# Kernel optimization log

Measured on AMD Instinct MI355X. Metric: run time of the kernel, lower is better.

The kernel has to match this reference:

```python
import jax, jax.numpy as jnp
import numpy as np

B, C, H, W = 32, 3, 224, 224
P = 16            # patch size
D = 768           # model dim
L = 12            # depth
HEADS = 12
DH = D // HEADS   # 64
MLP = 3072
NC = 1000
N = (H // P) * (W // P) + 1  # 197 tokens (196 patches + cls)


def setup_inputs() -> dict:
    key = jax.random.key(0)
    ks = iter(jax.random.split(key, 16))
    def rnd(shape, s=0.02):
        return jax.random.normal(next(ks), shape, dtype=jnp.float32) * s
    return dict(
        imgs=jax.random.normal(next(ks), (B, C, H, W), dtype=jnp.float32),
        patch_w=rnd((D, C, P, P)),
        patch_b=jnp.zeros((D,), jnp.float32),
        cls_token=rnd((D,)),
        pos_emb=rnd((N, D)),
        ln1_g=jnp.ones((L, D), jnp.float32), ln1_b=jnp.zeros((L, D), jnp.float32),
        wq=rnd((L, D, D)), bq=jnp.zeros((L, D), jnp.float32),
        wk=rnd((L, D, D)), bk=jnp.zeros((L, D), jnp.float32),
        wv=rnd((L, D, D)), bv=jnp.zeros((L, D), jnp.float32),
        wo=rnd((L, D, D)), bo=jnp.zeros((L, D), jnp.float32),
        ln2_g=jnp.ones((L, D), jnp.float32), ln2_b=jnp.zeros((L, D), jnp.float32),
        w1=rnd((L, D, MLP)), b1=jnp.zeros((L, MLP), jnp.float32),
        w2=rnd((L, MLP, D)), b2=jnp.zeros((L, D), jnp.float32),
        hn_g=jnp.ones((D,), jnp.float32), hn_b=jnp.zeros((D,), jnp.float32),
        hw=rnd((D, NC)), hb=jnp.zeros((NC,), jnp.float32),
    )


def layer_norm(x, g, b, eps=1e-5):
    mu = x.mean(-1, keepdims=True)
    var = ((x - mu) ** 2).mean(-1, keepdims=True)
    return (x - mu) * jax.lax.rsqrt(var + eps) * g + b


def reference(imgs, patch_w, patch_b, cls_token, pos_emb,
              ln1_g, ln1_b, wq, bq, wk, bk, wv, bv, wo, bo,
              ln2_g, ln2_b, w1, b1, w2, b2, hn_g, hn_b, hw, hb):
    # patch embedding: strided conv, NCHW / OIHW
    x = jax.lax.conv_general_dilated(
        imgs, patch_w, window_strides=(P, P), padding='VALID',
        dimension_numbers=('NCHW', 'OIHW', 'NCHW'))
    x = x + patch_b[None, :, None, None]
    x = x.reshape(B, D, -1).transpose(0, 2, 1)          # [B, 196, D]
    cls = jnp.broadcast_to(cls_token, (B, 1, D))        # zeros_like + cls_token
    x = jnp.concatenate([cls, x], axis=1) + pos_emb[:N] # [B, N, D]

    scale = DH ** -0.5
    for i in range(L):
        h = layer_norm(x, ln1_g[i], ln1_b[i])
        q = (h @ wq[i] + bq[i]).reshape(B, N, HEADS, DH)
        k = (h @ wk[i] + bk[i]).reshape(B, N, HEADS, DH)
        v = (h @ wv[i] + bv[i]).reshape(B, N, HEADS, DH)
        att = jax.nn.softmax(jnp.einsum('bnhd,bmhd->bhnm', q, k) * scale, axis=-1)
        o = jnp.einsum('bhnm,bmhd->bnhd', att, v).reshape(B, N, D)
        x = x + (o @ wo[i] + bo[i])
        h = layer_norm(x, ln2_g[i], ln2_b[i])
        x = x + (jax.nn.gelu(h @ w1[i] + b1[i]) @ w2[i] + b2[i])

    x = x.mean(axis=1)                                   # [B, D]
    return layer_norm(x, hn_g, hn_b) @ hw + hb           # [B, NC]
```

## Files before the change

kernel.cpp:

```cpp
#include <hip/hip_runtime.h>
#include <hip/hip_bf16.h>

typedef unsigned short u16;
typedef __bf16 bf16x8 __attribute__((ext_vector_type(8)));
typedef float f32x4 __attribute__((ext_vector_type(4)));

#define BATCH 32
#define NTOK 197
#define DIM 768
#define LAYERS 12
#define HEADS 12
#define DHEAD 64
#define MLPD 3072
#define NCLS 1000
#define SROWS 6304
#define SLD 224

constexpr long OFF_X  = 0;
constexpr long OFF_H  = 19365888;
constexpr long OFF_O  = 29048832;
constexpr long OFF_WB = 38731776;
constexpr long OFF_Q  = 43450368;
constexpr long OFF_K  = 53133312;
constexpr long OFF_VT = 62816256;
constexpr long OFF_S  = 73826304;
constexpr long OFF_PL = OFF_WB;
constexpr long OFF_HB = OFF_WB + 98304;

__device__ inline u16 f2bf(float f) {
    __hip_bfloat16 h = __float2bfloat16(f);
    return __builtin_bit_cast(u16, h);
}
__device__ inline float bf2f(u16 u) {
    unsigned int x = ((unsigned int)u) << 16;
    return __builtin_bit_cast(float, x);
}
__device__ inline void async16(const u16* g, u16* l) {
    __builtin_amdgcn_global_load_lds(
        (const __attribute__((address_space(1))) void*)g,
        (__attribute__((address_space(3))) void*)l, 16, 0, 0);
}

__global__ __launch_bounds__(256) void im2col_kernel(
        const float* __restrict__ imgs, u16* __restrict__ out) {
    int idx = blockIdx.x * 256 + threadIdx.x;
    if (idx >= 6272 * 768) return;
    int col = idx % 768, row = idx / 768;
    int b = row / 196, p = row % 196;
    int py = p / 14, px = p % 14;
    int c = col >> 8, ph = (col >> 4) & 15, pw = col & 15;
    float v = imgs[(((long)b * 3 + c) * 224 + (py * 16 + ph)) * 224 + (px * 16 + pw)];
    out[idx] = f2bf(v);
}

__global__ __launch_bounds__(256) void cast_kernel(
        const float* __restrict__ in, u16* __restrict__ out, int n) {
    int idx = blockIdx.x * 256 + threadIdx.x;
    if (idx < n) out[idx] = f2bf(in[idx]);
}

__global__ __launch_bounds__(256) void transpose_cast(
        const float* __restrict__ in, u16* __restrict__ out, int R, int C) {
    __shared__ float tile[32][33];
    int bx = blockIdx.x * 32;
    int by = blockIdx.y * 32;
    int tx = threadIdx.x & 31, ty = threadIdx.x >> 5;
#pragma unroll
    for (int i = 0; i < 32; i += 8) {
        int r = by + ty + i, c = bx + tx;
        if (r < R && c < C) tile[ty + i][tx] = in[(long)r * C + c];
    }
    __syncthreads();
#pragma unroll
    for (int i = 0; i < 32; i += 8) {
        int c = bx + ty + i, r = by + tx;
        if (r < R && c < C) out[(long)c * R + r] = f2bf(tile[tx][ty + i]);
    }
}

__global__ __launch_bounds__(256) void add_pos_kernel(
        float* __restrict__ x, const float* __restrict__ cls,
        const float* __restrict__ pos) {
    int idx = blockIdx.x * 256 + threadIdx.x;
    if (idx >= SROWS * DIM) return;
    int d = idx % DIM, row = idx / DIM, n = row % NTOK;
    if (n == 0) x[idx] = cls[d] + pos[d];
    else        x[idx] += pos[(long)n * DIM + d];
}

__device__ inline float block_sum(float v, float* red) {
#pragma unroll
    for (int off = 32; off; off >>= 1) v += __shfl_xor(v, off, 64);
    int w = threadIdx.x >> 6;
    if ((threadIdx.x & 63) == 0) red[w] = v;
    __syncthreads();
    float s = red[0] + red[1] + red[2] + red[3];
    __syncthreads();
    return s;
}

__global__ __launch_bounds__(256) void ln_kernel(
        const float* __restrict__ x, const float* __restrict__ g,
        const float* __restrict__ bt, u16* __restrict__ out) {
    __shared__ float red[4];
    long row = blockIdx.x;
    const float* xr = x + row * DIM;
    int t = threadIdx.x;
    float v0 = xr[t], v1 = xr[t + 256], v2 = xr[t + 512];
    float mean = block_sum(v0 + v1 + v2, red) * (1.f / 768.f);
    float d0 = v0 - mean, d1 = v1 - mean, d2 = v2 - mean;
    float var = block_sum(d0 * d0 + d1 * d1 + d2 * d2, red) * (1.f / 768.f);
    float rs = rsqrtf(var + 1e-5f);
    u16* o = out + row * DIM;
    o[t]       = f2bf(d0 * rs * g[t]       + bt[t]);
    o[t + 256] = f2bf(d1 * rs * g[t + 256] + bt[t + 256]);
    o[t + 512] = f2bf(d2 * rs * g[t + 512] + bt[t + 512]);
}

__global__ __launch_bounds__(256) void softmax_rows(u16* __restrict__ S) {
    int row = blockIdx.x * 4 + (threadIdx.x >> 6);
    int lane = threadIdx.x & 63;
    u16* p = S + (long)row * SLD;
    float v[4];
#pragma unroll
    for (int i = 0; i < 4; i++) {
        int c = lane + i * 64;
        v[i] = (c < NTOK) ? bf2f(p[c]) : -1e30f;
    }
    float mx = fmaxf(fmaxf(v[0], v[1]), fmaxf(v[2], v[3]));
#pragma unroll
    for (int off = 32; off; off >>= 1) mx = fmaxf(mx, __shfl_xor(mx, off, 64));
    float s = 0.f;
#pragma unroll
    for (int i = 0; i < 4; i++) {
        v[i] = (v[i] > -1e29f) ? __expf(v[i] - mx) : 0.f;
        s += v[i];
    }
#pragma unroll
    for (int off = 32; off; off >>= 1) s += __shfl_xor(s, off, 64);
    float inv = 1.f / s;
#pragma unroll
    for (int i = 0; i < 4; i++) {
        int c = lane + i * 64;
        if (c < NTOK) p[c] = f2bf(v[i] * inv);
    }
}

__global__ __launch_bounds__(256) void mean_pool_kernel(
        const float* __restrict__ x, float* __restrict__ pooled) {
    int idx = blockIdx.x * 256 + threadIdx.x;
    if (idx >= BATCH * DIM) return;
    int b = idx / DIM, d = idx % DIM;
    float s = 0.f;
    for (int n = 0; n < NTOK; n++) s += x[((long)b * NTOK + n) * DIM + d];
    pooled[idx] = s * (1.f / 197.f);
}

__global__ __launch_bounds__(256) void head_kernel(
        const u16* __restrict__ hx, const float* __restrict__ hw,
        const float* __restrict__ hb, float* __restrict__ out) {
    __shared__ float xr[DIM];
    int b = blockIdx.x;
    for (int i = threadIdx.x; i < DIM; i += 256) xr[i] = bf2f(hx[b * DIM + i]);
    __syncthreads();
    for (int c = threadIdx.x; c < NCLS; c += 256) {
        float s = hb[c];
        for (int d = 0; d < DIM; d++) s += xr[d] * hw[(long)d * NCLS + c];
        out[b * NCLS + c] = s;
    }
}

constexpr int OM_F32 = 0, OM_BF16 = 1, OM_PATCH = 2, OM_QK = 3, OM_VT = 4,
              OM_S = 5, OM_ATTN = 6;
constexpr int EPI_NONE = 0, EPI_GELU = 1;

template<int TM, int TN, int OUT_MODE, int EPI, bool RESID>
__global__ __launch_bounds__(256, 2) void gemm_async(
        const u16* __restrict__ Aall, const u16* __restrict__ Ball,
        void* __restrict__ Cptr, const float* __restrict__ bias,
        int M, int N, int K, int lda, int ldb, int ldc,
        long sA, long sB, float scale) {
    __shared__ u16 As[TM * 32];
    __shared__ u16 Bs[TN * 32];
    int g = blockIdx.z;
    const u16* A = Aall + (long)g * sA;
    const u16* B = Ball + (long)g * sB;
    int m0 = blockIdx.x * TM;
    int n0 = blockIdx.y * TN;
    int tid = threadIdx.x;
    int lane = tid & 63;
    int wave = tid >> 6;
    int wm, wn;
    if (TN == 128) { wm = (wave & 1) * 64; wn = (wave >> 1) * 64; }
    else           { wm = wave * 64;       wn = 0; }
    int lm = lane & 15;
    int lq = lane >> 4;

    f32x4 acc[4][4];
    const f32x4 z4 = {0.f, 0.f, 0.f, 0.f};
#pragma unroll
    for (int i = 0; i < 4; i++)
#pragma unroll
        for (int j = 0; j < 4; j++) acc[i][j] = z4;

    int rsub = lane >> 2;
    int ksub = (lane & 3) * 8;

    for (int k0 = 0; k0 < K; k0 += 32) {
#pragma unroll
        for (int c = 0; c < TM / 64; c++) {
            int row = c * 64 + wave * 16;
            int gr = m0 + row + rsub;
            gr = gr < M ? gr : M - 1;
            async16(A + (long)gr * lda + k0 + ksub, &As[row * 32]);
        }
#pragma unroll
        for (int c = 0; c < TN / 64; c++) {
            int row = c * 64 + wave * 16;
            int gn = n0 + row + rsub;
            gn = gn < N ? gn : N - 1;
            async16(B + (long)gn * ldb + k0 + ksub, &Bs[row * 32]);
        }
        __syncthreads();
        bf16x8 af[4], bfr[4];
#pragma unroll
        for (int i = 0; i < 4; i++)
            af[i] = *reinterpret_cast<const bf16x8*>(&As[(wm + i * 16 + lm) * 32 + lq * 8]);
#pragma unroll
        for (int i = 0; i < 4; i++)
            bfr[i] = *reinterpret_cast<const bf16x8*>(&Bs[(wn + i * 16 + lm) * 32 + lq * 8]);
#pragma unroll
        for (int mi = 0; mi < 4; mi++)
#pragma unroll
            for (int ni = 0; ni < 4; ni++)
                acc[mi][ni] = __builtin_amdgcn_mfma_f32_16x16x32_bf16(
                        af[mi], bfr[ni], acc[mi][ni], 0, 0, 0);
        __syncthreads();
    }

    int nlim = (OUT_MODE == OM_S) ? SLD : N;
#pragma unroll
    for (int mi = 0; mi < 4; mi++) {
#pragma unroll
        for (int ni = 0; ni < 4; ni++) {
#pragma unroll
            for (int r = 0; r < 4; r++) {
                int m = m0 + wm + mi * 16 + lq * 4 + r;
                int n = n0 + wn + ni * 16 + lm;
                if (m < M && n < nlim) {
                    float v = 0.f;
                    if (!(OUT_MODE == OM_S && n >= N)) {
                        v = acc[mi][ni][r] * scale;
                        if (bias) v += bias[n];
                        if (EPI == EPI_GELU) {
                            float u = v;
                            v = 0.5f * u * (1.f + tanhf(0.7978845608028654f *
                                                        (u + 0.044715f * u * u * u)));
                        }
                    }
                    if (OUT_MODE == OM_F32) {
                        float* Cf = (float*)Cptr;
                        long idx = (long)m * ldc + n;
                        if (RESID) v += Cf[idx];
                        Cf[idx] = v;
                    } else if (OUT_MODE == OM_BF16) {
                        ((u16*)Cptr)[(long)m * ldc + n] = f2bf(v);
                    } else if (OUT_MODE == OM_PATCH) {
                        int row = m + m / 196 + 1;
                        ((float*)Cptr)[(long)row * DIM + n] = v;
                    } else if (OUT_MODE == OM_QK) {
                        int b = m / NTOK, tok = m - b * NTOK;
                        int hh = n >> 6, dh = n & 63;
                        ((u16*)Cptr)[((((long)b * HEADS + hh) * NTOK + tok) << 6) + dh] = f2bf(v);
                    } else if (OUT_MODE == OM_VT) {
                        int b = m / NTOK, tok = m - b * NTOK;
                        int hh = n >> 6, dh = n & 63;
                        ((u16*)Cptr)[(((long)b * HEADS + hh) * 64 + dh) * SLD + tok] = f2bf(v);
                    } else if (OUT_MODE == OM_S) {
                        ((u16*)Cptr)[(long)g * (NTOK * SLD) + (long)m * SLD + n] = f2bf(v);
                    } else {
                        int b = g / HEADS, hh = g - b * HEADS;
                        ((u16*)Cptr)[((long)(b * NTOK + m)) * DIM + hh * 64 + n] = f2bf(v);
                    }
                }
            }
        }
    }
}

extern "C" void kernel_launch(void* const* d_in, const int* in_sizes, int n_in,
                              void* d_out, int out_size, void* d_ws, size_t ws_size,
                              hipStream_t stream) {
    const float* imgs    = (const float*)d_in[0];
    const float* patch_w = (const float*)d_in[1];
    const float* patch_b = (const float*)d_in[2];
    const float* cls_tok = (const float*)d_in[3];
    const float* pos_emb = (const float*)d_in[4];
    const float* ln1_g   = (const float*)d_in[5];
    const float* ln1_b   = (const float*)d_in[6];
    const float* wq      = (const float*)d_in[7];
    const float* bq      = (const float*)d_in[8];
    const float* wk      = (const float*)d_in[9];
    const float* bk      = (const float*)d_in[10];
    const float* wv      = (const float*)d_in[11];
    const float* bv      = (const float*)d_in[12];
    const float* wo      = (const float*)d_in[13];
    const float* bo      = (const float*)d_in[14];
    const float* ln2_g   = (const float*)d_in[15];
    const float* ln2_b   = (const float*)d_in[16];
    const float* w1      = (const float*)d_in[17];
    const float* b1      = (const float*)d_in[18];
    const float* w2      = (const float*)d_in[19];
    const float* b2      = (const float*)d_in[20];
    const float* hn_g    = (const float*)d_in[21];
    const float* hn_b    = (const float*)d_in[22];
    const float* hw      = (const float*)d_in[23];
    const float* hbias   = (const float*)d_in[24];

    char* ws = (char*)d_ws;
    float* x     = (float*)(ws + OFF_X);
    u16*   h     = (u16*)(ws + OFF_H);
    u16*   obuf  = (u16*)(ws + OFF_O);
    u16*   wbuf  = (u16*)(ws + OFF_WB);
    u16*   qbuf  = (u16*)(ws + OFF_Q);
    u16*   kbuf  = (u16*)(ws + OFF_K);
    u16*   vtbuf = (u16*)(ws + OFF_VT);
    u16*   Sbuf  = (u16*)(ws + OFF_S);
    u16*   patchA = (u16*)(ws + OFF_Q);
    u16*   mlph   = (u16*)(ws + OFF_Q);
    float* pooled = (float*)(ws + OFF_PL);
    u16*   hb16   = (u16*)(ws + OFF_HB);

    im2col_kernel<<<(6272 * 768 + 255) / 256, 256, 0, stream>>>(imgs, patchA);
    cast_kernel<<<(589824 + 255) / 256, 256, 0, stream>>>(patch_w, wbuf, 589824);
    gemm_async<128, 128, OM_PATCH, EPI_NONE, false><<<dim3(49, 6, 1), 256, 0, stream>>>(
        patchA, wbuf, x, patch_b, 6272, 768, 768, 768, 768, 768, 0, 0, 1.f);
    add_pos_kernel<<<(SROWS * DIM + 255) / 256, 256, 0, stream>>>(x, cls_tok, pos_emb);

    for (int l = 0; l < LAYERS; ++l) {
        const long wstride = (long)DIM * DIM;
        ln_kernel<<<SROWS, 256, 0, stream>>>(x, ln1_g + l * DIM, ln1_b + l * DIM, h);

        transpose_cast<<<dim3(24, 24), 256, 0, stream>>>(wq + l * wstride, wbuf, DIM, DIM);
        gemm_async<128, 128, OM_QK, EPI_NONE, false><<<dim3(50, 6, 1), 256, 0, stream>>>(
            h, wbuf, qbuf, bq + l * DIM, SROWS, DIM, DIM, DIM, DIM, 0, 0, 0, 1.f);
        transpose_cast<<<dim3(24, 24), 256, 0, stream>>>(wk + l * wstride, wbuf, DIM, DIM);
        gemm_async<128, 128, OM_QK, EPI_NONE, false><<<dim3(50, 6, 1), 256, 0, stream>>>(
            h, wbuf, kbuf, bk + l * DIM, SROWS, DIM, DIM, DIM, DIM, 0, 0, 0, 1.f);
        transpose_cast<<<dim3(24, 24), 256, 0, stream>>>(wv + l * wstride, wbuf, DIM, DIM);
        gemm_async<128, 128, OM_VT, EPI_NONE, false><<<dim3(50, 6, 1), 256, 0, stream>>>(
            h, wbuf, vtbuf, bv + l * DIM, SROWS, DIM, DIM, DIM, DIM, 0, 0, 0, 1.f);

        gemm_async<128, 128, OM_S, EPI_NONE, false><<<dim3(2, 2, 384), 256, 0, stream>>>(
            qbuf, kbuf, Sbuf, nullptr, NTOK, NTOK, DHEAD, DHEAD, DHEAD, 0,
            (long)NTOK * DHEAD, (long)NTOK * DHEAD, 0.125f);
        softmax_rows<<<(384 * NTOK) / 4, 256, 0, stream>>>(Sbuf);
        gemm_async<256, 64, OM_ATTN, EPI_NONE, false><<<dim3(1, 1, 384), 256, 0, stream>>>(
            Sbuf, vtbuf, obuf, nullptr, NTOK, DHEAD, SLD, SLD, SLD, 0,
            (long)NTOK * SLD, (long)64 * SLD, 1.f);

        transpose_cast<<<dim3(24, 24), 256, 0, stream>>>(wo + l * wstride, wbuf, DIM, DIM);
        gemm_async<128, 128, OM_F32, EPI_NONE, true><<<dim3(50, 6, 1), 256, 0, stream>>>(
            obuf, wbuf, x, bo + l * DIM, SROWS, DIM, DIM, DIM, DIM, DIM, 0, 0, 1.f);

        ln_kernel<<<SROWS, 256, 0, stream>>>(x, ln2_g + l * DIM, ln2_b + l * DIM, h);
        transpose_cast<<<dim3(96, 24), 256, 0, stream>>>(w1 + (long)l * DIM * MLPD, wbuf, DIM, MLPD);
        gemm_async<128, 128, OM_BF16, EPI_GELU, false><<<dim3(50, 24, 1), 256, 0, stream>>>(
            h, wbuf, mlph, b1 + l * MLPD, SROWS, MLPD, DIM, DIM, DIM, MLPD, 0, 0, 1.f);
        transpose_cast<<<dim3(24, 96), 256, 0, stream>>>(w2 + (long)l * MLPD * DIM, wbuf, MLPD, DIM);
        gemm_async<128, 128, OM_F32, EPI_NONE, true><<<dim3(50, 6, 1), 256, 0, stream>>>(
            mlph, wbuf, x, b2 + l * DIM, SROWS, DIM, MLPD, MLPD, MLPD, DIM, 0, 0, 1.f);
    }

    mean_pool_kernel<<<(BATCH * DIM + 255) / 256, 256, 0, stream>>>(x, pooled);
    ln_kernel<<<BATCH, 256, 0, stream>>>(pooled, hn_g, hn_b, hb16);
    head_kernel<<<BATCH, 256, 0, stream>>>(hb16, hw, hbias, (float*)d_out);
}
```

Before: 5.666 ms.

## Fuse attention into one kernel, merge QKV GEMM and weight transposes

Replaces the separate QK^T GEMM, softmax and PV GEMM with a single attention kernel that keeps scores and probabilities in LDS per 64-query tile, removing the bf16 score buffer round-trip through global memory. Q, K and V projections become one GEMM with N=2304 and a per-segment epilogue, and the four DxD weight transposes run in one launch. The head kernel is also split across more blocks. This cuts launches and memory traffic, at the cost of high LDS use per block (about 70KB) in the attention kernel, which may limit occupancy.

```diff
diff --git a/kernel.cpp b/kernel.cpp
--- a/kernel.cpp
+++ b/kernel.cpp
@@ -15,6 +15,7 @@
 #define NCLS 1000
 #define SROWS 6304
 #define SLD 224
+#define PLD 232
 
 constexpr long OFF_X  = 0;
 constexpr long OFF_H  = 19365888;
@@ -23,9 +24,9 @@
 constexpr long OFF_Q  = 43450368;
 constexpr long OFF_K  = 53133312;
 constexpr long OFF_VT = 62816256;
-constexpr long OFF_S  = 73826304;
 constexpr long OFF_PL = OFF_WB;
 constexpr long OFF_HB = OFF_WB + 98304;
+constexpr long QK_SEG = 4841472;
 
 __device__ inline u16 f2bf(float f) {
     __hip_bfloat16 h = __float2bfloat16(f);
@@ -62,8 +63,7 @@
 __global__ __launch_bounds__(256) void transpose_cast(
         const float* __restrict__ in, u16* __restrict__ out, int R, int C) {
     __shared__ float tile[32][33];
-    int bx = blockIdx.x * 32;
-    int by = blockIdx.y * 32;
+    int bx = blockIdx.x * 32, by = blockIdx.y * 32;
     int tx = threadIdx.x & 31, ty = threadIdx.x >> 5;
 #pragma unroll
     for (int i = 0; i < 32; i += 8) {
@@ -76,6 +76,25 @@
         int c = bx + ty + i, r = by + tx;
         if (r < R && c < C) out[(long)c * R + r] = f2bf(tile[tx][ty + i]);
     }
+}
+
+__global__ __launch_bounds__(256) void transpose_cast4(
+        const float* __restrict__ p0, const float* __restrict__ p1,
+        const float* __restrict__ p2, const float* __restrict__ p3,
+        u16* __restrict__ out) {
+    __shared__ float tile[32][33];
+    int z = blockIdx.z;
+    const float* in = z == 0 ? p0 : z == 1 ? p1 : z == 2 ? p2 : p3;
+    u16* o = out + (long)z * DIM * DIM;
+    int bx = blockIdx.x * 32, by = blockIdx.y * 32;
+    int tx = threadIdx.x & 31, ty = threadIdx.x >> 5;
+#pragma unroll
+    for (int i = 0; i < 32; i += 8)
+        tile[ty + i][tx] = in[(long)(by + ty + i) * DIM + bx + tx];
+    __syncthreads();
+#pragma unroll
+    for (int i = 0; i < 32; i += 8)
+        o[(long)(bx + ty + i) * DIM + by + tx] = f2bf(tile[tx][ty + i]);
 }
 
 __global__ __launch_bounds__(256) void add_pos_kernel(
@@ -117,35 +136,6 @@
     o[t + 512] = f2bf(d2 * rs * g[t + 512] + bt[t + 512]);
 }
 
-__global__ __launch_bounds__(256) void softmax_rows(u16* __restrict__ S) {
-    int row = blockIdx.x * 4 + (threadIdx.x >> 6);
-    int lane = threadIdx.x & 63;
-    u16* p = S + (long)row * SLD;
-    float v[4];
-#pragma unroll
-    for (int i = 0; i < 4; i++) {
-        int c = lane + i * 64;
-        v[i] = (c < NTOK) ? bf2f(p[c]) : -1e30f;
-    }
-    float mx = fmaxf(fmaxf(v[0], v[1]), fmaxf(v[2], v[3]));
-#pragma unroll
-    for (int off = 32; off; off >>= 1) mx = fmaxf(mx, __shfl_xor(mx, off, 64));
-    float s = 0.f;
-#pragma unroll
-    for (int i = 0; i < 4; i++) {
-        v[i] = (v[i] > -1e29f) ? __expf(v[i] - mx) : 0.f;
-        s += v[i];
-    }
-#pragma unroll
-    for (int off = 32; off; off >>= 1) s += __shfl_xor(s, off, 64);
-    float inv = 1.f / s;
-#pragma unroll
-    for (int i = 0; i < 4; i++) {
-        int c = lane + i * 64;
-        if (c < NTOK) p[c] = f2bf(v[i] * inv);
-    }
-}
-
 __global__ __launch_bounds__(256) void mean_pool_kernel(
         const float* __restrict__ x, float* __restrict__ pooled) {
     int idx = blockIdx.x * 256 + threadIdx.x;
@@ -163,36 +153,32 @@
     int b = blockIdx.x;
     for (int i = threadIdx.x; i < DIM; i += 256) xr[i] = bf2f(hx[b * DIM + i]);
     __syncthreads();
-    for (int c = threadIdx.x; c < NCLS; c += 256) {
+    int c = blockIdx.y * 256 + threadIdx.x;
+    if (c < NCLS) {
         float s = hb[c];
         for (int d = 0; d < DIM; d++) s += xr[d] * hw[(long)d * NCLS + c];
         out[b * NCLS + c] = s;
     }
 }
 
-constexpr int OM_F32 = 0, OM_BF16 = 1, OM_PATCH = 2, OM_QK = 3, OM_VT = 4,
-              OM_S = 5, OM_ATTN = 6;
+constexpr int OM_F32 = 0, OM_BF16 = 1, OM_PATCH = 2, OM_QKV = 3;
 constexpr int EPI_NONE = 0, EPI_GELU = 1;
 
-template<int TM, int TN, int OUT_MODE, int EPI, bool RESID>
+template<int OUT_MODE, int EPI, bool RESID>
 __global__ __launch_bounds__(256, 2) void gemm_async(
-        const u16* __restrict__ Aall, const u16* __restrict__ Ball,
+        const u16* __restrict__ A, const u16* __restrict__ B,
         void* __restrict__ Cptr, const float* __restrict__ bias,
-        int M, int N, int K, int lda, int ldb, int ldc,
-        long sA, long sB, float scale) {
-    __shared__ u16 As[TM * 32];
-    __shared__ u16 Bs[TN * 32];
-    int g = blockIdx.z;
-    const u16* A = Aall + (long)g * sA;
-    const u16* B = Ball + (long)g * sB;
-    int m0 = blockIdx.x * TM;
-    int n0 = blockIdx.y * TN;
+        const float* __restrict__ bias2, const float* __restrict__ bias3,
+        int M, int N, int K, int lda, int ldb, int ldc) {
+    __shared__ u16 As[128 * 32];
+    __shared__ u16 Bs[128 * 32];
+    int m0 = blockIdx.x * 128;
+    int n0 = blockIdx.y * 128;
     int tid = threadIdx.x;
     int lane = tid & 63;
     int wave = tid >> 6;
-    int wm, wn;
-    if (TN == 128) { wm = (wave & 1) * 64; wn = (wave >> 1) * 64; }
-    else           { wm = wave * 64;       wn = 0; }
+    int wm = (wave & 1) * 64;
+    int wn = (wave >> 1) * 64;
     int lm = lane & 15;
     int lq = lane >> 4;
 
@@ -208,17 +194,11 @@
 
     for (int k0 = 0; k0 < K; k0 += 32) {
 #pragma unroll
-        for (int c = 0; c < TM / 64; c++) {
+        for (int c = 0; c < 2; c++) {
             int row = c * 64 + wave * 16;
-            int gr = m0 + row + rsub;
-            gr = gr < M ? gr : M - 1;
+            int gr = m0 + row + rsub; gr = gr < M ? gr : M - 1;
             async16(A + (long)gr * lda + k0 + ksub, &As[row * 32]);
-        }
-#pragma unroll
-        for (int c = 0; c < TN / 64; c++) {
-            int row = c * 64 + wave * 16;
-            int gn = n0 + row + rsub;
-            gn = gn < N ? gn : N - 1;
+            int gn = n0 + row + rsub; gn = gn < N ? gn : N - 1;
             async16(B + (long)gn * ldb + k0 + ksub, &Bs[row * 32]);
         }
         __syncthreads();
@@ -238,7 +218,6 @@
         __syncthreads();
     }
 
-    int nlim = (OUT_MODE == OM_S) ? SLD : N;
 #pragma unroll
     for (int mi = 0; mi < 4; mi++) {
 #pragma unroll
@@ -247,45 +226,190 @@
             for (int r = 0; r < 4; r++) {
                 int m = m0 + wm + mi * 16 + lq * 4 + r;
                 int n = n0 + wn + ni * 16 + lm;
-                if (m < M && n < nlim) {
-                    float v = 0.f;
-                    if (!(OUT_MODE == OM_S && n >= N)) {
-                        v = acc[mi][ni][r] * scale;
+                if (m < M && n < N) {
+                    float v = acc[mi][ni][r];
+                    if (OUT_MODE == OM_QKV) {
+                        int seg = n >= 1536 ? 2 : (n >= 768 ? 1 : 0);
+                        int nn = n - seg * 768;
+                        const float* bp = seg == 0 ? bias : seg == 1 ? bias2 : bias3;
+                        v += bp[nn];
+                        int b = m / NTOK, tok = m - b * NTOK;
+                        int hh = nn >> 6, dh = nn & 63;
+                        u16* base = (u16*)Cptr;
+                        if (seg < 2)
+                            base[(long)seg * QK_SEG +
+                                 ((((long)b * HEADS + hh) * NTOK + tok) << 6) + dh] = f2bf(v);
+                        else
+                            base[2 * QK_SEG +
+                                 (((long)b * HEADS + hh) * 64 + dh) * SLD + tok] = f2bf(v);
+                    } else {
                         if (bias) v += bias[n];
                         if (EPI == EPI_GELU) {
                             float u = v;
                             v = 0.5f * u * (1.f + tanhf(0.7978845608028654f *
                                                         (u + 0.044715f * u * u * u)));
                         }
-                    }
-                    if (OUT_MODE == OM_F32) {
-                        float* Cf = (float*)Cptr;
-                        long idx = (long)m * ldc + n;
-                        if (RESID) v += Cf[idx];
-                        Cf[idx] = v;
-                    } else if (OUT_MODE == OM_BF16) {
-                        ((u16*)Cptr)[(long)m * ldc + n] = f2bf(v);
-                    } else if (OUT_MODE == OM_PATCH) {
-                        int row = m + m / 196 + 1;
-                        ((float*)Cptr)[(long)row * DIM + n] = v;
-                    } else if (OUT_MODE == OM_QK) {
-                        int b = m / NTOK, tok = m - b * NTOK;
-                        int hh = n >> 6, dh = n & 63;
-                        ((u16*)Cptr)[((((long)b * HEADS + hh) * NTOK + tok) << 6) + dh] = f2bf(v);
-                    } else if (OUT_MODE == OM_VT) {
-                        int b = m / NTOK, tok = m - b * NTOK;
-                        int hh = n >> 6, dh = n & 63;
-                        ((u16*)Cptr)[(((long)b * HEADS + hh) * 64 + dh) * SLD + tok] = f2bf(v);
-                    } else if (OUT_MODE == OM_S) {
-                        ((u16*)Cptr)[(long)g * (NTOK * SLD) + (long)m * SLD + n] = f2bf(v);
-                    } else {
-                        int b = g / HEADS, hh = g - b * HEADS;
-                        ((u16*)Cptr)[((long)(b * NTOK + m)) * DIM + hh * 64 + n] = f2bf(v);
+                        if (OUT_MODE == OM_F32) {
+                            float* Cf = (float*)Cptr;
+                            long idx = (long)m * ldc + n;
+                            if (RESID) v += Cf[idx];
+                            Cf[idx] = v;
+                        } else if (OUT_MODE == OM_BF16) {
+                            ((u16*)Cptr)[(long)m * ldc + n] = f2bf(v);
+                        } else {
+                            int row = m + m / 196 + 1;
+                            ((float*)Cptr)[(long)row * DIM + n] = v;
+                        }
                     }
                 }
             }
         }
     }
+}
+
+__global__ __launch_bounds__(256) void attn_fused(
+        const u16* __restrict__ qbuf, const u16* __restrict__ kbuf,
+        const u16* __restrict__ vtbuf, u16* __restrict__ obuf) {
+    __shared__ char smem[71680];
+    u16* As = (u16*)smem;
+    u16* Bs = (u16*)(smem + 8192);
+    u16* Vs = (u16*)(smem + 40960);
+    float* red = (float*)(smem + 69632);
+    u16* Ps = (u16*)smem;
+
+    int t = blockIdx.x, g = blockIdx.y;
+    int q0 = t * 64;
+    const u16* Q  = qbuf  + (long)g * NTOK * DHEAD;
+    const u16* Kp = kbuf  + (long)g * NTOK * DHEAD;
+    const u16* Vt = vtbuf + (long)g * DHEAD * SLD;
+    int tid = threadIdx.x, lane = tid & 63, wave = tid >> 6;
+    int lm = lane & 15, lq = lane >> 4;
+    int rsub = lane >> 2, ksub = (lane & 3) * 8;
+
+#pragma unroll
+    for (int kh = 0; kh < 2; kh++) {
+        int gr = q0 + wave * 16 + rsub; gr = gr < NTOK ? gr : NTOK - 1;
+        async16(Q + (long)gr * DHEAD + kh * 32 + ksub, &As[kh * 2048 + wave * 16 * 32]);
+#pragma unroll
+        for (int c = 0; c < 4; c++) {
+            int gk = c * 64 + wave * 16 + rsub; gk = gk < NTOK ? gk : NTOK - 1;
+            async16(Kp + (long)gk * DHEAD + kh * 32 + ksub,
+                    &Bs[kh * 8192 + (c * 64 + wave * 16) * 32]);
+        }
+    }
+#pragma unroll
+    for (int cc = 0; cc < 7; cc++) {
+        int c = cc * 4 + wave;
+        async16(Vt + c * 512 + lane * 8, &Vs[c * 512]);
+    }
+    __syncthreads();
+
+    f32x4 acc[4][4];
+    const f32x4 z4 = {0.f, 0.f, 0.f, 0.f};
+#pragma unroll
+    for (int i = 0; i < 4; i++)
+#pragma unroll
+        for (int j = 0; j < 4; j++) acc[i][j] = z4;
+#pragma unroll
+    for (int kh = 0; kh < 2; kh++) {
+        bf16x8 af[4], bfr[4];
+#pragma unroll
+        for (int mi = 0; mi < 4; mi++)
+            af[mi] = *reinterpret_cast<const bf16x8*>(
+                &As[kh * 2048 + (mi * 16 + lm) * 32 + lq * 8]);
+#pragma unroll
+        for (int ni = 0; ni < 4; ni++)
+            bfr[ni] = *reinterpret_cast<const bf16x8*>(
+                &Bs[kh * 8192 + (wave * 64 + ni * 16 + lm) * 32 + lq * 8]);
+#pragma unroll
+        for (int mi = 0; mi < 4; mi++)
+#pragma unroll
+            for (int ni = 0; ni < 4; ni++)
+                acc[mi][ni] = __builtin_amdgcn_mfma_f32_16x16x32_bf16(
+                        af[mi], bfr[ni], acc[mi][ni], 0, 0, 0);
+    }
+
+#pragma unroll
+    for (int mi = 0; mi < 4; mi++)
+#pragma unroll
+        for (int ni = 0; ni < 4; ni++) {
+            int n = wave * 64 + ni * 16 + lm;
+#pragma unroll
+            for (int r = 0; r < 4; r++)
+                acc[mi][ni][r] = (n < NTOK) ? acc[mi][ni][r] * 0.125f : -1e30f;
+        }
+#pragma unroll
+    for (int mi = 0; mi < 4; mi++)
+#pragma unroll
+        for (int r = 0; r < 4; r++) {
+            float mp = fmaxf(fmaxf(acc[mi][0][r], acc[mi][1][r]),
+                             fmaxf(acc[mi][2][r], acc[mi][3][r]));
+#pragma unroll
+            for (int o = 1; o < 16; o <<= 1) mp = fmaxf(mp, __shfl_xor(mp, o));
+            if (lm == 0) red[wave * 64 + mi * 16 + lq * 4 + r] = mp;
+        }
+    __syncthreads();
+#pragma unroll
+    for (int mi = 0; mi < 4; mi++)
+#pragma unroll
+        for (int r = 0; r < 4; r++) {
+            int row = mi * 16 + lq * 4 + r;
+            float M = fmaxf(fmaxf(red[row], red[64 + row]),
+                            fmaxf(red[128 + row], red[192 + row]));
+            float sp = 0.f;
+#pragma unroll
+            for (int ni = 0; ni < 4; ni++) {
+                float e = __expf(acc[mi][ni][r] - M);
+                acc[mi][ni][r] = e;
+                sp += e;
+            }
+#pragma unroll
+            for (int o = 1; o < 16; o <<= 1) sp += __shfl_xor(sp, o);
+            if (lm == 0) red[256 + wave * 64 + row] = sp;
+        }
+    __syncthreads();
+#pragma unroll
+    for (int mi = 0; mi < 4; mi++)
+#pragma unroll
+        for (int r = 0; r < 4; r++) {
+            int row = mi * 16 + lq * 4 + r;
+            float s = red[256 + row] + red[256 + 64 + row] +
+                      red[256 + 128 + row] + red[256 + 192 + row];
+            float inv = 1.f / s;
+#pragma unroll
+            for (int ni = 0; ni < 4; ni++) {
+                int n = wave * 64 + ni * 16 + lm;
+                if (n < PLD) Ps[row * PLD + n] = f2bf(acc[mi][ni][r] * inv);
+            }
+        }
+    __syncthreads();
+
+    f32x4 pacc[4];
+#pragma unroll
+    for (int i = 0; i < 4; i++) pacc[i] = z4;
+    for (int k0 = 0; k0 < SLD; k0 += 32) {
+        bf16x8 paf = *reinterpret_cast<const bf16x8*>(
+            &Ps[(wave * 16 + lm) * PLD + k0 + lq * 8]);
+        bf16x8 pbf[4];
+#pragma unroll
+        for (int ni = 0; ni < 4; ni++)
+            pbf[ni] = *reinterpret_cast<const bf16x8*>(
+                &Vs[(ni * 16 + lm) * SLD + k0 + lq * 8]);
+#pragma unroll
+        for (int ni = 0; ni < 4; ni++)
+            pacc[ni] = __builtin_amdgcn_mfma_f32_16x16x32_bf16(
+                    paf, pbf[ni], pacc[ni], 0, 0, 0);
+    }
+    int b = g / HEADS, hh = g - b * HEADS;
+#pragma unroll
+    for (int ni = 0; ni < 4; ni++)
+#pragma unroll
+        for (int r = 0; r < 4; r++) {
+            int tok = q0 + wave * 16 + lq * 4 + r;
+            if (tok < NTOK)
+                obuf[((long)(b * NTOK + tok)) * DIM + hh * 64 + ni * 16 + lm] =
+                    f2bf(pacc[ni][r]);
+        }
 }
 
 extern "C" void kernel_launch(void* const* d_in, const int* in_sizes, int n_in,
@@ -325,7 +449,6 @@
     u16*   qbuf  = (u16*)(ws + OFF_Q);
     u16*   kbuf  = (u16*)(ws + OFF_K);
     u16*   vtbuf = (u16*)(ws + OFF_VT);
-    u16*   Sbuf  = (u16*)(ws + OFF_S);
     u16*   patchA = (u16*)(ws + OFF_Q);
     u16*   mlph   = (u16*)(ws + OFF_Q);
     float* pooled = (float*)(ws + OFF_PL);
@@ -333,46 +456,39 @@
 
     im2col_kernel<<<(6272 * 768 + 255) / 256, 256, 0, stream>>>(imgs, patchA);
     cast_kernel<<<(589824 + 255) / 256, 256, 0, stream>>>(patch_w, wbuf, 589824);
-    gemm_async<128, 128, OM_PATCH, EPI_NONE, false><<<dim3(49, 6, 1), 256, 0, stream>>>(
-        patchA, wbuf, x, patch_b, 6272, 768, 768, 768, 768, 768, 0, 0, 1.f);
+    gemm_async<OM_PATCH, EPI_NONE, false><<<dim3(49, 6), 256, 0, stream>>>(
+        patchA, wbuf, x, patch_b, nullptr, nullptr, 6272, 768, 768, 768, 768, 768);
     add_pos_kernel<<<(SROWS * DIM + 255) / 256, 256, 0, stream>>>(x, cls_tok, pos_emb);
 
     for (int l = 0; l < LAYERS; ++l) {
         const long wstride = (long)DIM * DIM;
         ln_kernel<<<SROWS, 256, 0, stream>>>(x, ln1_g + l * DIM, ln1_b + l * DIM, h);
 
-        transpose_cast<<<dim3(24, 24), 256, 0, stream>>>(wq + l * wstride, wbuf, DIM, DIM);
-        gemm_async<128, 128, OM_QK, EPI_NONE, false><<<dim3(50, 6, 1), 256, 0, stream>>>(
-            h, wbuf, qbuf, bq + l * DIM, SROWS, DIM, DIM, DIM, DIM, 0, 0, 0, 1.f);
-        transpose_cast<<<dim3(24, 24), 256, 0, stream>>>(wk + l * wstride, wbuf, DIM, DIM);
-        gemm_async<128, 128, OM_QK, EPI_NONE, false><<<dim3(50, 6, 1), 256, 0, stream>>>(
-            h, wbuf, kbuf, bk + l * DIM, SROWS, DIM, DIM, DIM, DIM, 0, 0, 0, 1.f);
-        transpose_cast<<<dim3(24, 24), 256, 0, stream>>>(wv + l * wstride, wbuf, DIM, DIM);
-        gemm_async<128, 128, OM_VT, EPI_NONE, false><<<dim3(50, 6, 1), 256, 0, stream>>>(
-            h, wbuf, vtbuf, bv + l * DIM, SROWS, DIM, DIM, DIM, DIM, 0, 0, 0, 1.f);
-
-        gemm_async<128, 128, OM_S, EPI_NONE, false><<<dim3(2, 2, 384), 256, 0, stream>>>(
-            qbuf, kbuf, Sbuf, nullptr, NTOK, NTOK, DHEAD, DHEAD, DHEAD, 0,
-            (long)NTOK * DHEAD, (long)NTOK * DHEAD, 0.125f);
-        softmax_rows<<<(384 * NTOK) / 4, 256, 0, stream>>>(Sbuf);
-        gemm_async<256, 64, OM_ATTN, EPI_NONE, false><<<dim3(1, 1, 384), 256, 0, stream>>>(
-            Sbuf, vtbuf, obuf, nullptr, NTOK, DHEAD, SLD, SLD, SLD, 0,
-            (long)NTOK * SLD, (long)64 * SLD, 1.f);
-
-        transpose_cast<<<dim3(24, 24), 256, 0, stream>>>(wo + l * wstride, wbuf, DIM, DIM);
-        gemm_async<128, 128, OM_F32, EPI_NONE, true><<<dim3(50, 6, 1), 256, 0, stream>>>(
-            obuf, wbuf, x, bo + l * DIM, SROWS, DIM, DIM, DIM, DIM, DIM, 0, 0, 1.f);
+        transpose_cast4<<<dim3(24, 24, 4), 256, 0, stream>>>(
+            wq + l * wstride, wk + l * wstride, wv + l * wstride, wo + l * wstride, wbuf);
+
+        gemm_async<OM_QKV, EPI_NONE, false><<<dim3(50, 18), 256, 0, stream>>>(
+            h, wbuf, qbuf, bq + l * DIM, bk + l * DIM, bv + l * DIM,
+            SROWS, 2304, DIM, DIM, DIM, 0);
+
+        attn_fused<<<dim3(4, 384), 256, 0, stream>>>(qbuf, kbuf, vtbuf, obuf);
+
+        gemm_async<OM_F32, EPI_NONE, true><<<dim3(50, 6), 256, 0, stream>>>(
+            obuf, wbuf + 3L * DIM * DIM, x, bo + l * DIM, nullptr, nullptr,
+            SROWS, DIM, DIM, DIM, DIM, DIM);
 
         ln_kernel<<<SROWS, 256, 0, stream>>>(x, ln2_g + l * DIM, ln2_b + l * DIM, h);
         transpose_cast<<<dim3(96, 24), 256, 0, stream>>>(w1 + (long)l * DIM * MLPD, wbuf, DIM, MLPD);
-        gemm_async<128, 128, OM_BF16, EPI_GELU, false><<<dim3(50, 24, 1), 256, 0, stream>>>(
-            h, wbuf, mlph, b1 + l * MLPD, SROWS, MLPD, DIM, DIM, DIM, MLPD, 0, 0, 1.f);
+        gemm_async<OM_BF16, EPI_GELU, false><<<dim3(50, 24), 256, 0, stream>>>(
+            h, wbuf, mlph, b1 + l * MLPD, nullptr, nullptr,
+            SROWS, MLPD, DIM, DIM, DIM, MLPD);
         transpose_cast<<<dim3(24, 96), 256, 0, stream>>>(w2 + (long)l * MLPD * DIM, wbuf, MLPD, DIM);
-        gemm_async<128, 128, OM_F32, EPI_NONE, true><<<dim3(50, 6, 1), 256, 0, stream>>>(
-            mlph, wbuf, x, b2 + l * DIM, SROWS, DIM, MLPD, MLPD, MLPD, DIM, 0, 0, 1.f);
+        gemm_async<OM_F32, EPI_NONE, true><<<dim3(50, 6), 256, 0, stream>>>(
+            mlph, wbuf, x, b2 + l * DIM, nullptr, nullptr,
+            SROWS, DIM, MLPD, MLPD, MLPD, DIM);
     }
 
     mean_pool_kernel<<<(BATCH * DIM + 255) / 256, 256, 0, stream>>>(x, pooled);
     ln_kernel<<<BATCH, 256, 0, stream>>>(pooled, hn_g, hn_b, hb16);
-    head_kernel<<<BATCH, 256, 0, stream>>>(hb16, hw, hbias, (float*)d_out);
-}
+    head_kernel<<<dim3(32, 4), 256, 0, stream>>>(hb16, hw, hbias, (float*)d_out);
+}
```

Result: faster. 4.638 ms (-18.1%).
